# Optimization experiments

Measured on AMD Instinct MI355X. Metric: run time of the kernel, lower is better.

The kernel has to match this reference:

```python
import jax, jax.numpy as jnp
import numpy as np

N_NODES = 50000
N_EDGES = 800000
IN_DIM = 128
HID = 32
HEADS = 4


def _lin_init(key, fan_in, fan_out):
    k1, k2 = jax.random.split(key)
    s = 1.0 / np.sqrt(fan_in)
    W = jax.random.uniform(k1, (fan_in, fan_out), jnp.float32, -s, s)
    b = jax.random.uniform(k2, (fan_out,), jnp.float32, -s, s)
    return W, b


def setup_inputs() -> dict:
    key = jax.random.key(0)
    keys = jax.random.split(key, 12)
    x = jax.random.normal(keys[0], (N_NODES, IN_DIM), jnp.float32)
    edge_index = jax.random.randint(keys[1], (2, N_EDGES), 0, N_NODES, jnp.int64)

    # conv1: in_dim -> heads*hid (128 -> 4*32)
    Wq1, bq1 = _lin_init(keys[2], IN_DIM, HEADS * HID)
    Wk1, bk1 = _lin_init(keys[3], IN_DIM, HEADS * HID)
    Wv1, bv1 = _lin_init(keys[4], IN_DIM, HEADS * HID)
    Ws1, bs1 = _lin_init(keys[5], IN_DIM, HEADS * HID)
    # conv2: 128 -> 1*32
    Wq2, bq2 = _lin_init(keys[6], HEADS * HID, HID)
    Wk2, bk2 = _lin_init(keys[7], HEADS * HID, HID)
    Wv2, bv2 = _lin_init(keys[8], HEADS * HID, HID)
    Ws2, bs2 = _lin_init(keys[9], HEADS * HID, HID)
    # output linear: 32 -> 1
    Wo, bo = _lin_init(keys[10], HID, 1)

    return {
        "x": x, "edge_index": edge_index,
        "Wq1": Wq1, "bq1": bq1, "Wk1": Wk1, "bk1": bk1,
        "Wv1": Wv1, "bv1": bv1, "Ws1": Ws1, "bs1": bs1,
        "Wq2": Wq2, "bq2": bq2, "Wk2": Wk2, "bk2": bk2,
        "Wv2": Wv2, "bv2": bv2, "Ws2": Ws2, "bs2": bs2,
        "Wo": Wo, "bo": bo,
    }


def transformer_conv(x, edge_index, Wq, bq, Wk, bk, Wv, bv, Ws, bs, heads, d):
    # PyG TransformerConv (concat=True, root_weight=True, beta=False, no edge attr).
    n = x.shape[0]
    src, dst = edge_index[0], edge_index[1]  # message j(src) -> i(dst)
    q = (x @ Wq + bq).reshape(n, heads, d)
    k = (x @ Wk + bk).reshape(n, heads, d)
    v = (x @ Wv + bv).reshape(n, heads, d)
    # per-edge attention logits [E, heads]
    logits = (q[dst] * k[src]).sum(-1) / jnp.sqrt(jnp.float32(d))
    # segment softmax over incoming edges of each target node
    m = jax.ops.segment_max(logits, dst, num_segments=n)
    p = jnp.exp(logits - m[dst])
    denom = jax.ops.segment_sum(p, dst, num_segments=n)
    alpha = p / denom[dst]  # [E, heads]
    # weighted scatter-add of values
    msg = alpha[:, :, None] * v[src]  # [E, heads, d]
    aggr = jax.ops.segment_sum(msg, dst, num_segments=n).reshape(n, heads * d)
    return aggr + x @ Ws + bs  # root (skip) connection


def reference(x, edge_index,
              Wq1, bq1, Wk1, bk1, Wv1, bv1, Ws1, bs1,
              Wq2, bq2, Wk2, bk2, Wv2, bv2, Ws2, bs2,
              Wo, bo):
    h = transformer_conv(x, edge_index, Wq1, bq1, Wk1, bk1, Wv1, bv1, Ws1, bs1, HEADS, HID)
    h = jax.nn.relu(h)
    h = transformer_conv(h, edge_index, Wq2, bq2, Wk2, bk2, Wv2, bv2, Ws2, bs2, 1, HID)
    h = jax.nn.relu(h)
    g = h.mean(axis=0)  # [HID]
    return g @ Wo + bo  # [1]
```

## Files before the change

### kernel.cpp

```cpp
#include <hip/hip_runtime.h>
#include <math.h>

#define N_NODES 50000
#define N_EDGES 800000
#define NBK 196
#define BCAP 6144

typedef short short8 __attribute__((ext_vector_type(8)));
typedef float f32x4 __attribute__((ext_vector_type(4)));
typedef float f32x2 __attribute__((ext_vector_type(2)));

__device__ inline unsigned short f2bf(float v) {
  unsigned u = __float_as_uint(v);
  u += 0x7FFFu + ((u >> 16) & 1u);
  return (unsigned short)(u >> 16);
}
__device__ inline float bf2f(unsigned short b) {
  return __uint_as_float(((unsigned)b) << 16);
}
__device__ inline float bflo(unsigned u) { return __uint_as_float(u << 16); }
__device__ inline float bfhi(unsigned u) { return __uint_as_float(u & 0xFFFF0000u); }
__device__ inline unsigned char f2fp8(float v) {
  return (unsigned char)(__builtin_amdgcn_cvt_pk_fp8_f32(v, 0.f, 0, false) & 0xFF);
}
template <bool HI>
__device__ inline f32x2 fp8dec(unsigned u) {
  return __builtin_amdgcn_cvt_pk_f32_fp8(u, HI);
}

#define SCL 0.17677669529663687f

#define W1_B 256
#define W2_B 64
__global__ void prep_fused(const float* __restrict__ Wq1, const float* __restrict__ Wk1,
                           const float* __restrict__ Wv1, const float* __restrict__ Ws1,
                           const float* __restrict__ bq1, const float* __restrict__ bk1,
                           const float* __restrict__ bv1, const float* __restrict__ bs1,
                           const float* __restrict__ Wq2, const float* __restrict__ Wk2,
                           const float* __restrict__ Wv2, const float* __restrict__ Ws2,
                           const float* __restrict__ bq2, const float* __restrict__ bk2,
                           const float* __restrict__ bv2, const float* __restrict__ bs2,
                           unsigned short* __restrict__ Wt1, float* __restrict__ bcat1,
                           unsigned short* __restrict__ Wt2, float* __restrict__ bcat2,
                           const int* __restrict__ ei, int* __restrict__ bhist, int E) {
  const int b = blockIdx.x, tid = threadIdx.x;
  if (b < W1_B) {
    int i = b * 256 + tid;
    int c = i >> 7, k = i & 127;
    int mi = c >> 7, lc = c & 127;
    const float* W = (mi == 0) ? Wq1 : (mi == 1) ? Wk1 : (mi == 2) ? Wv1 : Ws1;
    float scl = (mi == 0) ? SCL : 1.f;
    Wt1[i] = f2bf(W[(size_t)k * 128 + lc] * scl);
    if (i < 512) {
      int bm = i >> 7, bl = i & 127;
      const float* bb = (bm == 0) ? bq1 : (bm == 1) ? bk1 : (bm == 2) ? bv1 : bs1;
      bcat1[i] = bb[bl] * ((bm == 0) ? SCL : 1.f);
    }
  } else if (b < W1_B + W2_B) {
    int i = (b - W1_B) * 256 + tid;
    int c = i >> 7, k = i & 127;
    int mi = c >> 5, lc = c & 31;
    const float* W = (mi == 0) ? Wq2 : (mi == 1) ? Wk2 : (mi == 2) ? Wv2 : Ws2;
    float scl = (mi == 0) ? SCL : 1.f;
    Wt2[i] = f2bf(W[(size_t)k * 32 + lc] * scl);
    if (i < 128) {
      int bm = i >> 5, bl = i & 31;
      const float* bb = (bm == 0) ? bq2 : (bm == 1) ? bk2 : (bm == 2) ? bv2 : bs2;
      bcat2[i] = bb[bl] * ((bm == 0) ? SCL : 1.f);
    }
  } else {
    __shared__ int h[NBK];
    for (int i = tid; i < NBK; i += 256) h[i] = 0;
    __syncthreads();
    int e = (b - W1_B - W2_B) * 4096 + tid;
#pragma unroll
    for (int p = 0; p < 16; ++p, e += 256)
      if (e < E) atomicAdd(&h[ei[E + e] >> 8], 1);
    __syncthreads();
    for (int i = tid; i < NBK; i += 256)
      if (h[i]) atomicAdd(&bhist[i], h[i]);
  }
}

__global__ void bucket_scan(const int* __restrict__ bhist, int* __restrict__ boff,
                            int* __restrict__ bcur) {
  __shared__ int s[256];
  int t = threadIdx.x;
  int v = (t < NBK) ? bhist[t] : 0;
  s[t] = v;
  __syncthreads();
#pragma unroll
  for (int off = 1; off < 256; off <<= 1) {
    int u = (t >= off) ? s[t - off] : 0;
    __syncthreads();
    s[t] += u;
    __syncthreads();
  }
  if (t < NBK) {
    int excl = s[t] - v;
    boff[t] = excl;
    bcur[t] = excl;
  }
  if (t == NBK - 1) boff[NBK] = s[t];
}

__global__ __launch_bounds__(256, 3) void scatter_gemm1(
    const int* __restrict__ ei, int* __restrict__ bcur, int* __restrict__ ebuck, int E, int EB,
    const float* __restrict__ X, const unsigned short* __restrict__ Wt,
    const float* __restrict__ bcat, unsigned short* __restrict__ Q1b,
    unsigned short* __restrict__ SK1, unsigned char* __restrict__ KV8, int M) {
  __shared__ __align__(16) unsigned char L[3][64 * 272];
  const int tid = threadIdx.x;

  if ((int)blockIdx.x < EB) {
    int* lh = (int*)L[0];
    for (int i = tid; i < NBK; i += 256) lh[i] = 0;
    __syncthreads();
    const int e0 = blockIdx.x * 4096;
    int pks[16], bks[16];
#pragma unroll
    for (int p = 0; p < 16; ++p) {
      int e = e0 + p * 256 + tid;
      if (e < E) {
        int src = ei[e], dst = ei[E + e];
        pks[p] = (src << 8) | (dst & 255);
        bks[p] = dst >> 8;
        atomicAdd(&lh[bks[p]], 1);
      } else bks[p] = -1;
    }
    __syncthreads();
    for (int i = tid; i < NBK; i += 256)
      if (lh[i]) lh[i] = atomicAdd(&bcur[i], lh[i]);
    __syncthreads();
#pragma unroll
    for (int p = 0; p < 16; ++p) {
      if (bks[p] >= 0) {
        int slot = atomicAdd(&lh[bks[p]], 1);
        ebuck[slot] = pks[p];
      }
    }
    return;
  }

  unsigned short* As = (unsigned short*)L[0];
  const int bm = (blockIdx.x - EB) * 64;
  const int wave = tid >> 6, lane = tid & 63;
  const int lr = lane & 15, q = lane >> 4;

#pragma unroll
  for (int p = 0; p < 8; ++p) {
    int f = tid + p * 256;
    int row = f >> 5, c4 = f & 31;
    int gm = bm + row; if (gm >= M) gm = 0;
    float4 v = *(const float4*)(X + (size_t)gm * 128 + c4 * 4);
    ushort4 o;
    o.x = f2bf(v.x); o.y = f2bf(v.y); o.z = f2bf(v.z); o.w = f2bf(v.w);
    *(ushort4*)&As[row * 136 + c4 * 4] = o;
  }
  __syncthreads();

#pragma unroll
  for (int pass = 0; pass < 2; ++pass) {
    const int colbase = pass * 256 + wave * 64;
    f32x4 acc[4][4];
#pragma unroll
    for (int i = 0; i < 4; ++i)
#pragma unroll
      for (int j = 0; j < 4; ++j) acc[i][j] = (f32x4){0.f, 0.f, 0.f, 0.f};

#pragma unroll
    for (int ks = 0; ks < 4; ++ks) {
      short8 af[4];
#pragma unroll
      for (int i = 0; i < 4; ++i)
        af[i] = *(short8*)&As[(i * 16 + lr) * 136 + ks * 32 + q * 8];
#pragma unroll
      for (int j = 0; j < 4; ++j) {
        short8 bf = *(const short8*)(Wt + (size_t)(colbase + j * 16 + lr) * 128 + ks * 32 + q * 8);
#pragma unroll
        for (int i = 0; i < 4; ++i)
          acc[i][j] = __builtin_amdgcn_mfma_f32_16x16x32_bf16(af[i], bf, acc[i][j], 0, 0, 0);
      }
    }

    float bj[4];
#pragma unroll
    for (int j = 0; j < 4; ++j) bj[j] = bcat[colbase + j * 16 + lr];

    if (pass == 0) {
      if (wave < 2) {
        unsigned short* Ls16 = (unsigned short*)L[1];
#pragma unroll
        for (int i = 0; i < 4; ++i)
#pragma unroll
          for (int r = 0; r < 4; ++r) {
            int row = i * 16 + q * 4 + r;
#pragma unroll
            for (int j = 0; j < 4; ++j)
              Ls16[row * 136 + wave * 64 + j * 16 + lr] = f2bf(acc[i][j][r] + bj[j]);
          }
      } else {
        unsigned char* KLs = L[2];
#pragma unroll
        for (int i = 0; i < 4; ++i)
#pragma unroll
          for (int r = 0; r < 4; ++r) {
            int row = i * 16 + q * 4 + r;
#pragma unroll
            for (int j = 0; j < 4; ++j) {
              int d = (wave - 2) * 64 + j * 16 + lr;
              KLs[row * 272 + 4 * (d >> 1) + (d & 1)] = f2fp8(acc[i][j][r] + bj[j]);
            }
          }
      }
    } else {
      __syncthreads();
      if (wave < 2) {
        unsigned char* KLs = L[2];
#pragma unroll
        for (int i = 0; i < 4; ++i)
#pragma unroll
          for (int r = 0; r < 4; ++r) {
            int row = i * 16 + q * 4 + r;
#pragma unroll
            for (int j = 0; j < 4; ++j) {
              int d = wave * 64 + j * 16 + lr;
              KLs[row * 272 + 4 * (d >> 1) + 2 + (d & 1)] = f2fp8(acc[i][j][r] + bj[j]);
            }
          }
      } else {
        unsigned short* Ls16 = (unsigned short*)L[0];
#pragma unroll
        for (int i = 0; i < 4; ++i)
#pragma unroll
          for (int r = 0; r < 4; ++r) {
            int row = i * 16 + q * 4 + r;
#pragma unroll
            for (int j = 0; j < 4; ++j)
              Ls16[row * 136 + (wave - 2) * 64 + j * 16 + lr] = f2bf(acc[i][j][r] + bj[j]);
          }
      }
    }
  }
  __syncthreads();

#pragma unroll
  for (int p = 0; p < 4; ++p) {
    int f = tid + p * 256;
    int row = f >> 4, u = f & 15;
    int gr = bm + row;
    if (gr < M) {
      *(uint4*)(Q1b + (size_t)gr * 128 + u * 8) = *(uint4*)&((unsigned short*)L[1])[row * 136 + u * 8];
      *(uint4*)(KV8 + (size_t)gr * 256 + u * 16) = *(uint4*)&L[2][row * 272 + u * 16];
      *(uint4*)(SK1 + (size_t)gr * 128 + u * 8) = *(uint4*)&((unsigned short*)L[0])[row * 136 + u * 8];
    }
  }
}

__global__ void bucket_csr(const int* __restrict__ ebuck, const int* __restrict__ boff,
                           int* __restrict__ rowptr, int* __restrict__ esrc, int N) {
  const int b = blockIdx.x;
  const int lo = boff[b], hi = boff[b + 1];
  const int cnt = hi - lo;
  __shared__ int hist[256];
  __shared__ int cur[256];
  __shared__ int sorted[BCAP];
  const int t = threadIdx.x;
  hist[t] = 0;
  __syncthreads();
  for (int i = t; i < cnt; i += 256) atomicAdd(&hist[ebuck[lo + i] & 255], 1);
  __syncthreads();
  int v = hist[t];
  sorted[t] = v;
  __syncthreads();
#pragma unroll
  for (int off = 1; off < 256; off <<= 1) {
    int u = (t >= off) ? sorted[t - off] : 0;
    __syncthreads();
    sorted[t] += u;
    __syncthreads();
  }
  int excl = sorted[t] - v;
  cur[t] = excl;
  int node = b * 256 + t;
  if (node <= N) rowptr[node] = lo + excl;
  __syncthreads();
  for (int i = t; i < cnt; i += 256) {
    int pk = ebuck[lo + i];
    int slot = atomicAdd(&cur[pk & 255], 1);
    if (slot < BCAP) sorted[slot] = pk;
    else esrc[lo + slot] = pk & 0xFFFFFF00;
  }
  __syncthreads();
  int lim = cnt < BCAP ? cnt : BCAP;
  for (int i = t; i < lim; i += 256) esrc[lo + i] = sorted[i] & 0xFFFFFF00;
}

__global__ __launch_bounds__(256) void gemm2(
    const unsigned short* __restrict__ Ab, const unsigned short* __restrict__ Wt,
    const float* __restrict__ bcat, unsigned char* __restrict__ C2b, int M) {
  __shared__ __align__(16) unsigned short As[64 * 136];
  __shared__ __align__(16) unsigned char Lsb[64 * 272];
  const int bm = blockIdx.x * 64;
  const int tid = threadIdx.x, wave = tid >> 6, lane = tid & 63;
  const int lr = lane & 15, q = lane >> 4;

#pragma unroll
  for (int p = 0; p < 4; ++p) {
    int f = tid + p * 256;
    int row = f >> 4, chunk = f & 15;
    int gm = bm + row; if (gm >= M) gm = 0;
    uint4 v = *(const uint4*)(Ab + (size_t)gm * 128 + chunk * 8);
    *(uint4*)&As[row * 136 + chunk * 8] = v;
  }
  __syncthreads();

  f32x4 acc[4][2];
#pragma unroll
  for (int i = 0; i < 4; ++i)
#pragma unroll
    for (int j = 0; j < 2; ++j) acc[i][j] = (f32x4){0.f, 0.f, 0.f, 0.f};

#pragma unroll
  for (int ks = 0; ks < 4; ++ks) {
    short8 af[4];
#pragma unroll
    for (int i = 0; i < 4; ++i)
      af[i] = *(short8*)&As[(i * 16 + lr) * 136 + ks * 32 + q * 8];
#pragma unroll
    for (int j = 0; j < 2; ++j) {
      short8 bf = *(const short8*)(Wt + (size_t)(wave * 32 + j * 16 + lr) * 128 + ks * 32 + q * 8);
#pragma unroll
      for (int i = 0; i < 4; ++i)
        acc[i][j] = __builtin_amdgcn_mfma_f32_16x16x32_bf16(af[i], bf, acc[i][j], 0, 0, 0);
    }
  }

  float bj[2];
#pragma unroll
  for (int j = 0; j < 2; ++j) bj[j] = bcat[wave * 32 + j * 16 + lr];
#pragma unroll
  for (int i = 0; i < 4; ++i)
#pragma unroll
    for (int r = 0; r < 4; ++r) {
      int row = i * 16 + q * 4 + r;
#pragma unroll
      for (int j = 0; j < 2; ++j) {
        int c = wave * 32 + j * 16 + lr;
        float val = acc[i][j][r] + bj[j];
        if (c < 32) {
          *(unsigned short*)&Lsb[row * 272 + 2 * c] = f2bf(val);
        } else if (c < 64) {
          int d = c - 32;
          Lsb[row * 272 + 64 + 4 * (d >> 1) + (d & 1)] = f2fp8(val);
        } else if (c < 96) {
          int d = c - 64;
          Lsb[row * 272 + 64 + 4 * (d >> 1) + 2 + (d & 1)] = f2fp8(val);
        } else {
          *(unsigned short*)&Lsb[row * 272 + 192 + 2 * (c - 96)] = f2bf(val);
        }
      }
    }
  __syncthreads();
#pragma unroll
  for (int p = 0; p < 16; ++p) {
    int idx = tid + p * 256;
    int row = idx >> 6, u = idx & 63;
    int gr = bm + row;
    if (gr < M) *(unsigned*)(C2b + (size_t)gr * 256 + u * 4) = *(const unsigned*)&Lsb[row * 272 + u * 4];
  }
}

__global__ void node_attn1(const int* __restrict__ rowptr, const int* __restrict__ esrc,
                           const unsigned short* __restrict__ Qb,
                           const unsigned char* __restrict__ KV8,
                           const unsigned short* __restrict__ SK, unsigned short* __restrict__ Hb,
                           int n) {
  int node = (blockIdx.x * blockDim.x + threadIdx.x) >> 6;
  int lane = threadIdx.x & 63;
  if (node >= n) return;
  const int g = lane >> 4, ll = lane & 15;
  const int r0 = rowptr[node], r1 = rowptr[node + 1];
  uint4 qq = *(const uint4*)(Qb + (size_t)node * 128 + ll * 8);
  const float q0 = bflo(qq.x), q1 = bfhi(qq.x), q2 = bflo(qq.y), q3 = bfhi(qq.y);
  const float q4 = bflo(qq.z), q5 = bfhi(qq.z), q6 = bflo(qq.w), q7 = bfhi(qq.w);
  float l = 0.f;
  float a0 = 0.f, a1 = 0.f, a2 = 0.f, a3 = 0.f, a4 = 0.f, a5 = 0.f, a6 = 0.f, a7 = 0.f;
  const unsigned char* kvb = KV8 + ll * 16;
  int j = r0;
  for (; j + 8 <= r1; j += 8) {
    int e = j + g * 2;
    int sA = esrc[e], sB = esrc[e + 1];
    uint4 uA = *(const uint4*)(kvb + sA);
    uint4 uB = *(const uint4*)(kvb + sB);
    f32x2 kA0 = fp8dec<false>(uA.x), kA1 = fp8dec<false>(uA.y),
          kA2 = fp8dec<false>(uA.z), kA3 = fp8dec<false>(uA.w);
    f32x2 kB0 = fp8dec<false>(uB.x), kB1 = fp8dec<false>(uB.y),
          kB2 = fp8dec<false>(uB.z), kB3 = fp8dec<false>(uB.w);
    float dA = q0 * kA0.x + q1 * kA0.y + q2 * kA1.x + q3 * kA1.y
             + q4 * kA2.x + q5 * kA2.y + q6 * kA3.x + q7 * kA3.y;
    float dB = q0 * kB0.x + q1 * kB0.y + q2 * kB1.x + q3 * kB1.y
             + q4 * kB2.x + q5 * kB2.y + q6 * kB3.x + q7 * kB3.y;
#pragma unroll
    for (int msk = 1; msk <= 2; msk <<= 1) {
      dA += __shfl_xor(dA, msk);
      dB += __shfl_xor(dB, msk);
    }
    float pA = __expf(dA), pB = __expf(dB);
    l += pA + pB;
    f32x2 vA0 = fp8dec<true>(uA.x), vA1 = fp8dec<true>(uA.y),
          vA2 = fp8dec<true>(uA.z), vA3 = fp8dec<true>(uA.w);
    f32x2 vB0 = fp8dec<true>(uB.x), vB1 = fp8dec<true>(uB.y),
          vB2 = fp8dec<true>(uB.z), vB3 = fp8dec<true>(uB.w);
    a0 += pA * vA0.x + pB * vB0.x;
    a1 += pA * vA0.y + pB * vB0.y;
    a2 += pA * vA1.x + pB * vB1.x;
    a3 += pA * vA1.y + pB * vB1.y;
    a4 += pA * vA2.x + pB * vB2.x;
    a5 += pA * vA2.y + pB * vB2.y;
    a6 += pA * vA3.x + pB * vB3.x;
    a7 += pA * vA3.y + pB * vB3.y;
  }
  for (; j < r1; j += 4) {
    int e = j + g;
    bool v = e < r1;
    int s = esrc[v ? e : r0];
    uint4 u = *(const uint4*)(kvb + s);
    f32x2 k0 = fp8dec<false>(u.x), k1 = fp8dec<false>(u.y),
          k2 = fp8dec<false>(u.z), k3 = fp8dec<false>(u.w);
    float d = q0 * k0.x + q1 * k0.y + q2 * k1.x + q3 * k1.y
            + q4 * k2.x + q5 * k2.y + q6 * k3.x + q7 * k3.y;
#pragma unroll
    for (int msk = 1; msk <= 2; msk <<= 1) d += __shfl_xor(d, msk);
    float p = v ? __expf(d) : 0.f;
    l += p;
    f32x2 v0 = fp8dec<true>(u.x), v1 = fp8dec<true>(u.y),
          v2 = fp8dec<true>(u.z), v3 = fp8dec<true>(u.w);
    a0 += p * v0.x; a1 += p * v0.y; a2 += p * v1.x; a3 += p * v1.y;
    a4 += p * v2.x; a5 += p * v2.y; a6 += p * v3.x; a7 += p * v3.y;
  }
#pragma unroll
  for (int msk = 16; msk <= 32; msk <<= 1) {
    l  += __shfl_xor(l, msk);
    a0 += __shfl_xor(a0, msk);
    a1 += __shfl_xor(a1, msk);
    a2 += __shfl_xor(a2, msk);
    a3 += __shfl_xor(a3, msk);
    a4 += __shfl_xor(a4, msk);
    a5 += __shfl_xor(a5, msk);
    a6 += __shfl_xor(a6, msk);
    a7 += __shfl_xor(a7, msk);
  }
  float inv = (l > 0.f) ? 1.f / l : 0.f;
  if (g == 0) {
    uint4 sk = *(const uint4*)(SK + (size_t)node * 128 + ll * 8);
    float o0 = fmaxf(bflo(sk.x) + a0 * inv, 0.f);
    float o1 = fmaxf(bfhi(sk.x) + a1 * inv, 0.f);
    float o2 = fmaxf(bflo(sk.y) + a2 * inv, 0.f);
    float o3 = fmaxf(bfhi(sk.y) + a3 * inv, 0.f);
    float o4 = fmaxf(bflo(sk.z) + a4 * inv, 0.f);
    float o5 = fmaxf(bfhi(sk.z) + a5 * inv, 0.f);
    float o6 = fmaxf(bflo(sk.w) + a6 * inv, 0.f);
    float o7 = fmaxf(bfhi(sk.w) + a7 * inv, 0.f);
    uint4 hb;
    hb.x = ((unsigned)f2bf(o1) << 16) | (unsigned)f2bf(o0);
    hb.y = ((unsigned)f2bf(o3) << 16) | (unsigned)f2bf(o2);
    hb.z = ((unsigned)f2bf(o5) << 16) | (unsigned)f2bf(o4);
    hb.w = ((unsigned)f2bf(o7) << 16) | (unsigned)f2bf(o6);
    *(uint4*)(Hb + (size_t)node * 128 + ll * 8) = hb;
  }
}

__global__ void node_attn2(const int* __restrict__ rowptr, const int* __restrict__ esrc,
                           const unsigned char* __restrict__ C2b, const float* __restrict__ Wo,
                           float* __restrict__ pblock, int n) {
  __shared__ float ps[4];
  int node = (blockIdx.x * blockDim.x + threadIdx.x) >> 6;
  int lane = threadIdx.x & 63;
  int wave = threadIdx.x >> 6;
  const int g = lane >> 3, gl = lane & 7;
  float t = 0.f;
  if (node < n) {
    const int r0 = rowptr[node], r1 = rowptr[node + 1];
    uint2 qu = *(const uint2*)(C2b + (size_t)node * 256 + gl * 8);
    const float q0 = bflo(qu.x), q1 = bfhi(qu.x), q2 = bflo(qu.y), q3 = bfhi(qu.y);
    float l = 0.f, a0 = 0.f, a1 = 0.f, a2 = 0.f, a3 = 0.f;
    const unsigned char* kvb = C2b + 64 + gl * 8;
    int j = r0;
    for (; j + 8 <= r1; j += 8) {
      int s = esrc[j + g];
      uint2 u = *(const uint2*)(kvb + s);
      f32x2 k0 = fp8dec<false>(u.x), k1 = fp8dec<false>(u.y);
      float d = q0 * k0.x + q1 * k0.y + q2 * k1.x + q3 * k1.y;
#pragma unroll
      for (int msk = 1; msk <= 4; msk <<= 1) d += __shfl_xor(d, msk);
      float p = __expf(d);
      l += p;
      f32x2 v0 = fp8dec<true>(u.x), v1 = fp8dec<true>(u.y);
      a0 += p * v0.x; a1 += p * v0.y; a2 += p * v1.x; a3 += p * v1.y;
    }
    for (; j < r1; j += 8) {
      bool v = (j + g) < r1;
      int s = esrc[v ? j + g : r0];
      uint2 u = *(const uint2*)(kvb + s);
      f32x2 kd0 = fp8dec<false>(u.x), kd1 = fp8dec<false>(u.y);
      float d = q0 * kd0.x + q1 * kd0.y + q2 * kd1.x + q3 * kd1.y;
#pragma unroll
      for (int msk = 1; msk <= 4; msk <<= 1) d += __shfl_xor(d, msk);
      float p = v ? __expf(d) : 0.f;
      l += p;
      f32x2 vd0 = fp8dec<true>(u.x), vd1 = fp8dec<true>(u.y);
      a0 += p * vd0.x; a1 += p * vd0.y; a2 += p * vd1.x; a3 += p * vd1.y;
    }
#pragma unroll
    for (int msk = 8; msk <= 32; msk <<= 1) {
      l  += __shfl_xor(l, msk);
      a0 += __shfl_xor(a0, msk);
      a1 += __shfl_xor(a1, msk);
      a2 += __shfl_xor(a2, msk);
      a3 += __shfl_xor(a3, msk);
    }
    float inv = (l > 0.f) ? 1.f / l : 0.f;
    uint2 hu = *(const uint2*)(C2b + (size_t)node * 256 + 192 + gl * 8);
    float o0 = fmaxf(bflo(hu.x) + a0 * inv, 0.f);
    float o1 = fmaxf(bfhi(hu.x) + a1 * inv, 0.f);
    float o2 = fmaxf(bflo(hu.y) + a2 * inv, 0.f);
    float o3 = fmaxf(bfhi(hu.y) + a3 * inv, 0.f);
    t = o0 * Wo[4 * gl] + o1 * Wo[4 * gl + 1] + o2 * Wo[4 * gl + 2] + o3 * Wo[4 * gl + 3];
#pragma unroll
    for (int msk = 1; msk <= 4; msk <<= 1) t += __shfl_xor(t, msk);
  }
  if (lane == 0) ps[wave] = t;
  __syncthreads();
  if (threadIdx.x == 0) pblock[blockIdx.x] = ps[0] + ps[1] + ps[2] + ps[3];
}

__global__ void final_out(const float* __restrict__ pblock, const float* __restrict__ bo,
                          float* __restrict__ out, int nb, float invN) {
  __shared__ float s[256];
  float acc = 0.f;
  for (int i = threadIdx.x; i < nb; i += 256) acc += pblock[i];
  s[threadIdx.x] = acc;
  __syncthreads();
  for (int off = 128; off >= 1; off >>= 1) {
    if (threadIdx.x < off) s[threadIdx.x] += s[threadIdx.x + off];
    __syncthreads();
  }
  if (threadIdx.x == 0) out[0] = s[0] * invN + bo[0];
}

extern "C" void kernel_launch(void* const* d_in, const int* in_sizes, int n_in,
                              void* d_out, int out_size, void* d_ws, size_t ws_size,
                              hipStream_t stream) {
  const float* x   = (const float*)d_in[0];
  const int*   ei  = (const int*)d_in[1];
  const float* Wq1 = (const float*)d_in[2];  const float* bq1 = (const float*)d_in[3];
  const float* Wk1 = (const float*)d_in[4];  const float* bk1 = (const float*)d_in[5];
  const float* Wv1 = (const float*)d_in[6];  const float* bv1 = (const float*)d_in[7];
  const float* Ws1 = (const float*)d_in[8];  const float* bs1 = (const float*)d_in[9];
  const float* Wq2 = (const float*)d_in[10]; const float* bq2 = (const float*)d_in[11];
  const float* Wk2 = (const float*)d_in[12]; const float* bk2 = (const float*)d_in[13];
  const float* Wv2 = (const float*)d_in[14]; const float* bv2 = (const float*)d_in[15];
  const float* Ws2 = (const float*)d_in[16]; const float* bs2 = (const float*)d_in[17];
  const float* Wo  = (const float*)d_in[18]; const float* bo  = (const float*)d_in[19];

  char* ws = (char*)d_ws;
  const int N = N_NODES, E = N_EDGES;
  const int GB = (N + 63) / 64;
  const int EB = (E + 4095) / 4096;
  const int AB = (N * 64) / 256;

  unsigned short* Q1b = (unsigned short*)(ws + 0);
  unsigned short* SK1 = (unsigned short*)(ws + 12800000);
  unsigned char*  KV1 = (unsigned char*)(ws + 25600000);
  unsigned short* H1b = (unsigned short*)(ws + 51200000);
  unsigned char*  C2  = (unsigned char*)(ws + 64000000);
  int* rowptr = (int*)(ws + 89600000);
  int* esrc   = (int*)(ws + 89900032);
  int* bhist  = (int*)(ws + 93100032);
  int* boff   = (int*)(ws + 93101056);
  int* bcur   = (int*)(ws + 93102080);
  unsigned short* Wt1   = (unsigned short*)(ws + 93103104);
  unsigned short* Wt2   = (unsigned short*)(ws + 93234176);
  float*          bcat1 = (float*)(ws + 93266944);
  float*          bcat2 = (float*)(ws + 93268992);
  float*          pblock = (float*)(ws + 93269504);
  int*            ebuck = (int*)(ws + 93319552);

  float* out = (float*)d_out;

  dim3 blk(256);

  hipMemsetAsync(bhist, 0, NBK * sizeof(int), stream);

  prep_fused<<<dim3(W1_B + W2_B + EB), blk, 0, stream>>>(
      Wq1, Wk1, Wv1, Ws1, bq1, bk1, bv1, bs1,
      Wq2, Wk2, Wv2, Ws2, bq2, bk2, bv2, bs2,
      Wt1, bcat1, Wt2, bcat2, ei, bhist, E);

  bucket_scan<<<dim3(1), blk, 0, stream>>>(bhist, boff, bcur);

  scatter_gemm1<<<dim3(EB + GB), blk, 0, stream>>>(
      ei, bcur, ebuck, E, EB, x, Wt1, bcat1, Q1b, SK1, KV1, N);

  bucket_csr<<<dim3(NBK), blk, 0, stream>>>(ebuck, boff, rowptr, esrc, N);

  node_attn1<<<dim3(AB), blk, 0, stream>>>(rowptr, esrc, Q1b, KV1, SK1, H1b, N);

  gemm2<<<dim3(GB), blk, 0, stream>>>(H1b, Wt2, bcat2, C2, N);

  node_attn2<<<dim3(AB), blk, 0, stream>>>(rowptr, esrc, C2, Wo, pblock, N);

  final_out<<<dim3(1), blk, 0, stream>>>(pblock, bo, out, AB, 1.0f / (float)N);
}
```

Before: 240.7 us.

## Regroup preprocessing kernels to fold bucket scan and overlap CSR build with GEMM1

The bucket scan kernel is removed. Each scatter block now recomputes the prefix scan from the histogram, and bcur becomes a zero-based counter added to the scanned bucket base. Weight conversion moves into the scatter kernel, and the per-bucket CSR sort is merged into the GEMM1 launch so the two run concurrently in one grid. This cuts one launch and lets CSR construction overlap with GEMM1. The cost is that every block repeats the scan, and the first GEMM1 now has to wait for a separate histogram kernel to finish.

After: 245.0 us. Within noise of the previous version (+1.8%).

```diff
diff --git a/kernel.cpp b/kernel.cpp
--- a/kernel.cpp
+++ b/kernel.cpp
@@ -29,94 +29,55 @@
 }
 
 #define SCL 0.17677669529663687f
-
 #define W1_B 256
 #define W2_B 64
-__global__ void prep_fused(const float* __restrict__ Wq1, const float* __restrict__ Wk1,
-                           const float* __restrict__ Wv1, const float* __restrict__ Ws1,
-                           const float* __restrict__ bq1, const float* __restrict__ bk1,
-                           const float* __restrict__ bv1, const float* __restrict__ bs1,
-                           const float* __restrict__ Wq2, const float* __restrict__ Wk2,
-                           const float* __restrict__ Wv2, const float* __restrict__ Ws2,
-                           const float* __restrict__ bq2, const float* __restrict__ bk2,
-                           const float* __restrict__ bv2, const float* __restrict__ bs2,
-                           unsigned short* __restrict__ Wt1, float* __restrict__ bcat1,
-                           unsigned short* __restrict__ Wt2, float* __restrict__ bcat2,
-                           const int* __restrict__ ei, int* __restrict__ bhist, int E) {
+
+__global__ void edge_hist(const int* __restrict__ ei, int* __restrict__ bhist, int E) {
+  __shared__ int h[NBK];
+  const int tid = threadIdx.x;
+  for (int i = tid; i < NBK; i += 256) h[i] = 0;
+  __syncthreads();
+  int e = blockIdx.x * 4096 + tid;
+#pragma unroll
+  for (int p = 0; p < 16; ++p, e += 256)
+    if (e < E) atomicAdd(&h[ei[E + e] >> 8], 1);
+  __syncthreads();
+  for (int i = tid; i < NBK; i += 256)
+    if (h[i]) atomicAdd(&bhist[i], h[i]);
+}
+
+__global__ void scatter_w(const int* __restrict__ ei, const int* __restrict__ bhist,
+                          int* __restrict__ bcur, int* __restrict__ ebuck, int E, int EB,
+                          const float* __restrict__ Wq1, const float* __restrict__ Wk1,
+                          const float* __restrict__ Wv1, const float* __restrict__ Ws1,
+                          const float* __restrict__ bq1, const float* __restrict__ bk1,
+                          const float* __restrict__ bv1, const float* __restrict__ bs1,
+                          const float* __restrict__ Wq2, const float* __restrict__ Wk2,
+                          const float* __restrict__ Wv2, const float* __restrict__ Ws2,
+                          const float* __restrict__ bq2, const float* __restrict__ bk2,
+                          const float* __restrict__ bv2, const float* __restrict__ bs2,
+                          unsigned short* __restrict__ Wt1, float* __restrict__ bcat1,
+                          unsigned short* __restrict__ Wt2, float* __restrict__ bcat2) {
   const int b = blockIdx.x, tid = threadIdx.x;
-  if (b < W1_B) {
-    int i = b * 256 + tid;
-    int c = i >> 7, k = i & 127;
-    int mi = c >> 7, lc = c & 127;
-    const float* W = (mi == 0) ? Wq1 : (mi == 1) ? Wk1 : (mi == 2) ? Wv1 : Ws1;
-    float scl = (mi == 0) ? SCL : 1.f;
-    Wt1[i] = f2bf(W[(size_t)k * 128 + lc] * scl);
-    if (i < 512) {
-      int bm = i >> 7, bl = i & 127;
-      const float* bb = (bm == 0) ? bq1 : (bm == 1) ? bk1 : (bm == 2) ? bv1 : bs1;
-      bcat1[i] = bb[bl] * ((bm == 0) ? SCL : 1.f);
-    }
-  } else if (b < W1_B + W2_B) {
-    int i = (b - W1_B) * 256 + tid;
-    int c = i >> 7, k = i & 127;
-    int mi = c >> 5, lc = c & 31;
-    const float* W = (mi == 0) ? Wq2 : (mi == 1) ? Wk2 : (mi == 2) ? Wv2 : Ws2;
-    float scl = (mi == 0) ? SCL : 1.f;
-    Wt2[i] = f2bf(W[(size_t)k * 32 + lc] * scl);
-    if (i < 128) {
-      int bm = i >> 5, bl = i & 31;
-      const float* bb = (bm == 0) ? bq2 : (bm == 1) ? bk2 : (bm == 2) ? bv2 : bs2;
-      bcat2[i] = bb[bl] * ((bm == 0) ? SCL : 1.f);
-    }
-  } else {
-    __shared__ int h[NBK];
-    for (int i = tid; i < NBK; i += 256) h[i] = 0;
-    __syncthreads();
-    int e = (b - W1_B - W2_B) * 4096 + tid;
-#pragma unroll
-    for (int p = 0; p < 16; ++p, e += 256)
-      if (e < E) atomicAdd(&h[ei[E + e] >> 8], 1);
-    __syncthreads();
-    for (int i = tid; i < NBK; i += 256)
-      if (h[i]) atomicAdd(&bhist[i], h[i]);
-  }
-}
-
-__global__ void bucket_scan(const int* __restrict__ bhist, int* __restrict__ boff,
-                            int* __restrict__ bcur) {
-  __shared__ int s[256];
-  int t = threadIdx.x;
-  int v = (t < NBK) ? bhist[t] : 0;
-  s[t] = v;
-  __syncthreads();
-#pragma unroll
-  for (int off = 1; off < 256; off <<= 1) {
-    int u = (t >= off) ? s[t - off] : 0;
-    __syncthreads();
-    s[t] += u;
-    __syncthreads();
-  }
-  if (t < NBK) {
-    int excl = s[t] - v;
-    boff[t] = excl;
-    bcur[t] = excl;
-  }
-  if (t == NBK - 1) boff[NBK] = s[t];
-}
-
-__global__ __launch_bounds__(256, 3) void scatter_gemm1(
-    const int* __restrict__ ei, int* __restrict__ bcur, int* __restrict__ ebuck, int E, int EB,
-    const float* __restrict__ X, const unsigned short* __restrict__ Wt,
-    const float* __restrict__ bcat, unsigned short* __restrict__ Q1b,
-    unsigned short* __restrict__ SK1, unsigned char* __restrict__ KV8, int M) {
-  __shared__ __align__(16) unsigned char L[3][64 * 272];
-  const int tid = threadIdx.x;
-
-  if ((int)blockIdx.x < EB) {
-    int* lh = (int*)L[0];
-    for (int i = tid; i < NBK; i += 256) lh[i] = 0;
-    __syncthreads();
-    const int e0 = blockIdx.x * 4096;
+  if (b < EB) {
+    __shared__ int sc[256];
+    __shared__ int bl[256];
+    __shared__ int lh[256];
+    const int t = tid;
+    int v = (t < NBK) ? bhist[t] : 0;
+    sc[t] = v;
+    __syncthreads();
+#pragma unroll
+    for (int off = 1; off < 256; off <<= 1) {
+      int u = (t >= off) ? sc[t - off] : 0;
+      __syncthreads();
+      sc[t] += u;
+      __syncthreads();
+    }
+    bl[t] = sc[t] - v;
+    lh[t] = 0;
+    __syncthreads();
+    const int e0 = b * 4096;
     int pks[16], bks[16];
 #pragma unroll
     for (int p = 0; p < 16; ++p) {
@@ -130,7 +91,7 @@
     }
     __syncthreads();
     for (int i = tid; i < NBK; i += 256)
-      if (lh[i]) lh[i] = atomicAdd(&bcur[i], lh[i]);
+      if (lh[i]) lh[i] = bl[i] + atomicAdd(&bcur[i], lh[i]);
     __syncthreads();
 #pragma unroll
     for (int p = 0; p < 16; ++p) {
@@ -141,9 +102,98 @@
     }
     return;
   }
-
-  unsigned short* As = (unsigned short*)L[0];
-  const int bm = (blockIdx.x - EB) * 64;
+  const int b2 = b - EB;
+  if (b2 < W1_B) {
+    int i = b2 * 256 + tid;
+    int c = i >> 7, k = i & 127;
+    int mi = c >> 7, lc = c & 127;
+    const float* W = (mi == 0) ? Wq1 : (mi == 1) ? Wk1 : (mi == 2) ? Wv1 : Ws1;
+    float scl = (mi == 0) ? SCL : 1.f;
+    Wt1[i] = f2bf(W[(size_t)k * 128 + lc] * scl);
+    if (i < 512) {
+      int bm = i >> 7, blx = i & 127;
+      const float* bb = (bm == 0) ? bq1 : (bm == 1) ? bk1 : (bm == 2) ? bv1 : bs1;
+      bcat1[i] = bb[blx] * ((bm == 0) ? SCL : 1.f);
+    }
+  } else {
+    int i = (b2 - W1_B) * 256 + tid;
+    int c = i >> 7, k = i & 127;
+    int mi = c >> 5, lc = c & 31;
+    const float* W = (mi == 0) ? Wq2 : (mi == 1) ? Wk2 : (mi == 2) ? Wv2 : Ws2;
+    float scl = (mi == 0) ? SCL : 1.f;
+    Wt2[i] = f2bf(W[(size_t)k * 32 + lc] * scl);
+    if (i < 128) {
+      int bm = i >> 5, blx = i & 31;
+      const float* bb = (bm == 0) ? bq2 : (bm == 1) ? bk2 : (bm == 2) ? bv2 : bs2;
+      bcat2[i] = bb[blx] * ((bm == 0) ? SCL : 1.f);
+    }
+  }
+}
+
+__global__ __launch_bounds__(256, 3) void csr_gemm1(
+    const int* __restrict__ ebuck, const int* __restrict__ bhist,
+    int* __restrict__ rowptr, int* __restrict__ esrc, int N,
+    const float* __restrict__ X, const unsigned short* __restrict__ Wt,
+    const float* __restrict__ bcat, unsigned short* __restrict__ Q1b,
+    unsigned short* __restrict__ SK1, unsigned char* __restrict__ KV8, int M) {
+  __shared__ __align__(16) unsigned char L[3 * 64 * 272];
+  const int tid = threadIdx.x;
+
+  if ((int)blockIdx.x < NBK) {
+    int* s_scan = (int*)L;
+    int* hv     = (int*)(L + 1024);
+    int* hist   = (int*)(L + 2048);
+    int* cur    = (int*)(L + 3072);
+    int* sorted = (int*)(L + 4096);
+    const int b = blockIdx.x, t = tid;
+    int v = (t < NBK) ? bhist[t] : 0;
+    hv[t] = v;
+    s_scan[t] = v;
+    __syncthreads();
+#pragma unroll
+    for (int off = 1; off < 256; off <<= 1) {
+      int u = (t >= off) ? s_scan[t - off] : 0;
+      __syncthreads();
+      s_scan[t] += u;
+      __syncthreads();
+    }
+    const int lo = s_scan[b] - hv[b], hi = s_scan[b];
+    const int cnt = hi - lo;
+    hist[t] = 0;
+    __syncthreads();
+    for (int i = t; i < cnt; i += 256) atomicAdd(&hist[ebuck[lo + i] & 255], 1);
+    __syncthreads();
+    int v2 = hist[t];
+    sorted[t] = v2;
+    __syncthreads();
+#pragma unroll
+    for (int off = 1; off < 256; off <<= 1) {
+      int u = (t >= off) ? sorted[t - off] : 0;
+      __syncthreads();
+      sorted[t] += u;
+      __syncthreads();
+    }
+    int excl = sorted[t] - v2;
+    cur[t] = excl;
+    int node = b * 256 + t;
+    if (node <= N) rowptr[node] = lo + excl;
+    __syncthreads();
+    for (int i = t; i < cnt; i += 256) {
+      int pk = ebuck[lo + i];
+      int slot = atomicAdd(&cur[pk & 255], 1);
+      if (slot < BCAP) sorted[slot] = pk;
+      else esrc[lo + slot] = pk & 0xFFFFFF00;
+    }
+    __syncthreads();
+    int lim = cnt < BCAP ? cnt : BCAP;
+    for (int i = t; i < lim; i += 256) esrc[lo + i] = sorted[i] & 0xFFFFFF00;
+    return;
+  }
+
+  unsigned short* As = (unsigned short*)L;
+  unsigned short* L1 = (unsigned short*)(L + 17408);
+  unsigned char*  L2 = L + 34816;
+  const int bm = (blockIdx.x - NBK) * 64;
   const int wave = tid >> 6, lane = tid & 63;
   const int lr = lane & 15, q = lane >> 4;
 
@@ -189,7 +239,6 @@
 
     if (pass == 0) {
       if (wave < 2) {
-        unsigned short* Ls16 = (unsigned short*)L[1];
 #pragma unroll
         for (int i = 0; i < 4; ++i)
 #pragma unroll
@@ -197,10 +246,9 @@
             int row = i * 16 + q * 4 + r;
 #pragma unroll
             for (int j = 0; j < 4; ++j)
-              Ls16[row * 136 + wave * 64 + j * 16 + lr] = f2bf(acc[i][j][r] + bj[j]);
+              L1[row * 136 + wave * 64 + j * 16 + lr] = f2bf(acc[i][j][r] + bj[j]);
           }
       } else {
-        unsigned char* KLs = L[2];
 #pragma unroll
         for (int i = 0; i < 4; ++i)
 #pragma unroll
@@ -209,14 +257,13 @@
 #pragma unroll
             for (int j = 0; j < 4; ++j) {
               int d = (wave - 2) * 64 + j * 16 + lr;
-              KLs[row * 272 + 4 * (d >> 1) + (d & 1)] = f2fp8(acc[i][j][r] + bj[j]);
+              L2[row * 272 + 4 * (d >> 1) + (d & 1)] = f2fp8(acc[i][j][r] + bj[j]);
             }
           }
       }
     } else {
       __syncthreads();
       if (wave < 2) {
-        unsigned char* KLs = L[2];
 #pragma unroll
         for (int i = 0; i < 4; ++i)
 #pragma unroll
@@ -225,11 +272,10 @@
 #pragma unroll
             for (int j = 0; j < 4; ++j) {
               int d = wave * 64 + j * 16 + lr;
-              KLs[row * 272 + 4 * (d >> 1) + 2 + (d & 1)] = f2fp8(acc[i][j][r] + bj[j]);
+              L2[row * 272 + 4 * (d >> 1) + 2 + (d & 1)] = f2fp8(acc[i][j][r] + bj[j]);
             }
           }
       } else {
-        unsigned short* Ls16 = (unsigned short*)L[0];
 #pragma unroll
         for (int i = 0; i < 4; ++i)
 #pragma unroll
@@ -237,7 +283,7 @@
             int row = i * 16 + q * 4 + r;
 #pragma unroll
             for (int j = 0; j < 4; ++j)
-              Ls16[row * 136 + (wave - 2) * 64 + j * 16 + lr] = f2bf(acc[i][j][r] + bj[j]);
+              As[row * 136 + (wave - 2) * 64 + j * 16 + lr] = f2bf(acc[i][j][r] + bj[j]);
           }
       }
     }
@@ -250,50 +296,11 @@
     int row = f >> 4, u = f & 15;
     int gr = bm + row;
     if (gr < M) {
-      *(uint4*)(Q1b + (size_t)gr * 128 + u * 8) = *(uint4*)&((unsigned short*)L[1])[row * 136 + u * 8];
-      *(uint4*)(KV8 + (size_t)gr * 256 + u * 16) = *(uint4*)&L[2][row * 272 + u * 16];
-      *(uint4*)(SK1 + (size_t)gr * 128 + u * 8) = *(uint4*)&((unsigned short*)L[0])[row * 136 + u * 8];
-    }
-  }
-}
-
-__global__ void bucket_csr(const int* __restrict__ ebuck, const int* __restrict__ boff,
-                           int* __restrict__ rowptr, int* __restrict__ esrc, int N) {
-  const int b = blockIdx.x;
-  const int lo = boff[b], hi = boff[b + 1];
-  const int cnt = hi - lo;
-  __shared__ int hist[256];
-  __shared__ int cur[256];
-  __shared__ int sorted[BCAP];
-  const int t = threadIdx.x;
-  hist[t] = 0;
-  __syncthreads();
-  for (int i = t; i < cnt; i += 256) atomicAdd(&hist[ebuck[lo + i] & 255], 1);
-  __syncthreads();
-  int v = hist[t];
-  sorted[t] = v;
-  __syncthreads();
-#pragma unroll
-  for (int off = 1; off < 256; off <<= 1) {
-    int u = (t >= off) ? sorted[t - off] : 0;
-    __syncthreads();
-    sorted[t] += u;
-    __syncthreads();
-  }
-  int excl = sorted[t] - v;
-  cur[t] = excl;
-  int node = b * 256 + t;
-  if (node <= N) rowptr[node] = lo + excl;
-  __syncthreads();
-  for (int i = t; i < cnt; i += 256) {
-    int pk = ebuck[lo + i];
-    int slot = atomicAdd(&cur[pk & 255], 1);
-    if (slot < BCAP) sorted[slot] = pk;
-    else esrc[lo + slot] = pk & 0xFFFFFF00;
-  }
-  __syncthreads();
-  int lim = cnt < BCAP ? cnt : BCAP;
-  for (int i = t; i < lim; i += 256) esrc[lo + i] = sorted[i] & 0xFFFFFF00;
+      *(uint4*)(Q1b + (size_t)gr * 128 + u * 8) = *(uint4*)&L1[row * 136 + u * 8];
+      *(uint4*)(KV8 + (size_t)gr * 256 + u * 16) = *(uint4*)&L2[row * 272 + u * 16];
+      *(uint4*)(SK1 + (size_t)gr * 128 + u * 8) = *(uint4*)&As[row * 136 + u * 8];
+    }
+  }
 }
 
 __global__ __launch_bounds__(256) void gemm2(
@@ -578,8 +585,7 @@
   int* rowptr = (int*)(ws + 89600000);
   int* esrc   = (int*)(ws + 89900032);
   int* bhist  = (int*)(ws + 93100032);
-  int* boff   = (int*)(ws + 93101056);
-  int* bcur   = (int*)(ws + 93102080);
+  int* bcur   = (int*)(ws + 93101056);
   unsigned short* Wt1   = (unsigned short*)(ws + 93103104);
   unsigned short* Wt2   = (unsigned short*)(ws + 93234176);
   float*          bcat1 = (float*)(ws + 93266944);
@@ -591,19 +597,18 @@
 
   dim3 blk(256);
 
-  hipMemsetAsync(bhist, 0, NBK * sizeof(int), stream);
-
-  prep_fused<<<dim3(W1_B + W2_B + EB), blk, 0, stream>>>(
+  hipMemsetAsync(bhist, 0, 2048, stream);
+
+  edge_hist<<<dim3(EB), blk, 0, stream>>>(ei, bhist, E);
+
+  scatter_w<<<dim3(EB + W1_B + W2_B), blk, 0, stream>>>(
+      ei, bhist, bcur, ebuck, E, EB,
       Wq1, Wk1, Wv1, Ws1, bq1, bk1, bv1, bs1,
       Wq2, Wk2, Wv2, Ws2, bq2, bk2, bv2, bs2,
-      Wt1, bcat1, Wt2, bcat2, ei, bhist, E);
-
-  bucket_scan<<<dim3(1), blk, 0, stream>>>(bhist, boff, bcur);
-
-  scatter_gemm1<<<dim3(EB + GB), blk, 0, stream>>>(
-      ei, bcur, ebuck, E, EB, x, Wt1, bcat1, Q1b, SK1, KV1, N);
-
-  bucket_csr<<<dim3(NBK), blk, 0, stream>>>(ebuck, boff, rowptr, esrc, N);
+      Wt1, bcat1, Wt2, bcat2);
+
+  csr_gemm1<<<dim3(NBK + GB), blk, 0, stream>>>(
+      ebuck, bhist, rowptr, esrc, N, x, Wt1, bcat1, Q1b, SK1, KV1, N);
 
   node_attn1<<<dim3(AB), blk, 0, stream>>>(rowptr, esrc, Q1b, KV1, SK1, H1b, N);
 
```
